# Kernel optimization log

Hardware: AMD Instinct MI355X
Metric: run time of the kernel (lower is better)

The kernel has to match this reference:

```python
import jax, jax.numpy as jnp
import numpy as np

S_DIM, I_DIM, O_DIM = 1024, 2048, 1024
TOTAL = S_DIM + I_DIM + O_DIM  # 4096
INPUT_DIM, NUM_CLASSES, BATCH = 2048, 1000, 256


def setup_inputs() -> dict:
    key = jax.random.key(0)
    ks = jax.random.split(key, 6)
    x = jax.random.normal(ks[0], (BATCH, INPUT_DIM), dtype=jnp.float32)
    W = jax.random.normal(ks[1], (TOTAL, TOTAL), dtype=jnp.float32) * 0.02
    # torch Linear: weight [out, in], bias [out]
    in_w = jax.random.normal(ks[2], (S_DIM, INPUT_DIM), dtype=jnp.float32) * (1.0 / np.sqrt(INPUT_DIM))
    in_b = jax.random.normal(ks[3], (S_DIM,), dtype=jnp.float32) * 0.01
    out_w = jax.random.normal(ks[4], (NUM_CLASSES, O_DIM), dtype=jnp.float32) * (1.0 / np.sqrt(O_DIM))
    out_b = jax.random.normal(ks[5], (NUM_CLASSES,), dtype=jnp.float32) * 0.01
    return {"x": x, "W": W, "in_w": in_w, "in_b": in_b, "out_w": out_w, "out_b": out_b, "time_steps": 10}


def reference(x, W, in_w, in_b, out_w, out_b, time_steps):
    B = x.shape[0]
    S, I, O = S_DIM, I_DIM, O_DIM
    # slice effective W into 9 sub-blocks (use_lora=False -> W_eff = W)
    W_ss, W_sr, W_so = W[:S, :S], W[:S, S:S + I], W[:S, S + I:]
    W_rs, W_rr, W_ro = W[S:S + I, :S], W[S:S + I, S:S + I], W[S:S + I, S + I:]
    W_os, W_or, W_oo = W[S + I:, :S], W[S + I:, S:S + I], W[S + I:, S + I:]

    E = x @ in_w.T + in_b  # [B, S]
    gate = (jnp.arange(time_steps) % 5 == 0).astype(x.dtype)  # E injected when t%5==0

    init = (jnp.zeros((B, S), x.dtype), jnp.zeros((B, I), x.dtype), jnp.zeros((B, O), x.dtype))

    def step(carry, g):
        Ss, Is, Os = carry
        S_next = jax.nn.relu(Ss @ W_ss + g * E + Is @ W_rs + Os @ W_os)
        I_next = jax.nn.relu(Is @ W_rr + Ss @ W_sr + Os @ W_or)
        O_next = jax.nn.relu(Os @ W_oo + Is @ W_ro + Ss @ W_so)
        return (S_next, I_next, O_next), None

    (Ss, Is, Os), _ = jax.lax.scan(step, init, gate)
    return Os @ out_w.T + out_b  # [B, num_classes]
```

## Files before the change

### kernel.cpp

```cpp
#include <hip/hip_runtime.h>


typedef __bf16 bf16x8 __attribute__((ext_vector_type(8)));
typedef float  f32x16 __attribute__((ext_vector_type(16)));

#define TOTAL 4096
#define BATCH 256
#define INDIM 2048
#define SDIM  1024
#define NCLS  1000

#define MFMA(a, b, c) __builtin_amdgcn_mfma_f32_32x32x16_bf16((a), (b), (c), 0, 0, 0)

__device__ inline f32x16 zero16() {
    f32x16 v;
#pragma unroll
    for (int i = 0; i < 16; ++i) v[i] = 0.f;
    return v;
}

__device__ inline void swz_slot(const float* __restrict__ in, __bf16* __restrict__ out,
                                int C, int Rvalid, int t) {
    const int lane = t & 63;
    const int frag = t >> 6;
    const int kcN = C >> 4;
    const int rt = frag / kcN;
    const int kc = frag - rt * kcN;
    const int r = rt * 32 + (lane & 31);
    const int c = kc * 16 + (lane >> 5) * 8;
    alignas(16) __bf16 v[8];
    if (r < Rvalid) {
        const float* p = in + (size_t)r * C + c;
#pragma unroll
        for (int j = 0; j < 8; ++j) v[j] = (__bf16)p[j];
    } else {
#pragma unroll
        for (int j = 0; j < 8; ++j) v[j] = (__bf16)0.f;
    }
    *(ulonglong2*)(out + (size_t)t * 8) = *(const ulonglong2*)v;
}

__global__ __launch_bounds__(256) void k_prep(const float* __restrict__ W,
                                              const float* __restrict__ x,
                                              const float* __restrict__ in_w,
                                              const float* __restrict__ in_b,
                                              const float* __restrict__ out_w,
                                              __bf16* __restrict__ WT,
                                              __bf16* __restrict__ OWT,
                                              float* __restrict__ Ebuf,
                                              __bf16* __restrict__ H0) {
    __shared__ float t[16 * 512];
    const int bid = blockIdx.x;
    const int tid = threadIdx.x;
    if (bid < 256) {
        float* red = t;
        const int mt = bid >> 5, nt = bid & 31;
        const int wave = tid >> 6, lane = tid & 63;
        const int l31 = lane & 31, kh = (lane >> 5) * 8;
        const int k0 = wave * 512;
        const float* Ax = x    + (size_t)(mt * 32 + l31) * INDIM + k0 + kh;
        const float* Bw = in_w + (size_t)(nt * 32 + l31) * INDIM + k0 + kh;
        f32x16 acc = zero16();
#pragma unroll 4
        for (int i = 0; i < 32; ++i) {
            const float* pa = Ax + i * 16;
            const float* pb = Bw + i * 16;
            float4 a0 = *(const float4*)pa, a1 = *(const float4*)(pa + 4);
            float4 b0 = *(const float4*)pb, b1 = *(const float4*)(pb + 4);
            bf16x8 a, b;
            a[0] = (__bf16)a0.x; a[1] = (__bf16)a0.y; a[2] = (__bf16)a0.z; a[3] = (__bf16)a0.w;
            a[4] = (__bf16)a1.x; a[5] = (__bf16)a1.y; a[6] = (__bf16)a1.z; a[7] = (__bf16)a1.w;
            b[0] = (__bf16)b0.x; b[1] = (__bf16)b0.y; b[2] = (__bf16)b0.z; b[3] = (__bf16)b0.w;
            b[4] = (__bf16)b1.x; b[5] = (__bf16)b1.y; b[6] = (__bf16)b1.z; b[7] = (__bf16)b1.w;
            acc = MFMA(a, b, acc);
        }
#pragma unroll
        for (int r = 0; r < 16; ++r) {
            int row = (r & 3) + 8 * (r >> 2) + 4 * (lane >> 5);
            red[wave * 1024 + row * 32 + l31] = acc[r];
        }
        __syncthreads();
        const int e0 = tid * 4;
        float4 s = {0.f, 0.f, 0.f, 0.f};
#pragma unroll
        for (int w = 0; w < 4; ++w) {
            float4 v = *(const float4*)&red[w * 1024 + e0];
            s.x += v.x; s.y += v.y; s.z += v.z; s.w += v.w;
        }
        const int row = e0 >> 5, col = e0 & 31;
        const int m = mt * 32 + row, n = nt * 32 + col;
        float v[4] = {s.x + in_b[n], s.y + in_b[n + 1], s.z + in_b[n + 2], s.w + in_b[n + 3]};
        *(float4*)(Ebuf + m * SDIM + n) = *(const float4*)v;
        alignas(8) __bf16 o[4];
#pragma unroll
        for (int j = 0; j < 4; ++j) o[j] = (__bf16)fmaxf(v[j], 0.f);
        const size_t frag = (size_t)(m >> 5) * (TOTAL / 16) + (n >> 4);
        const int lh = (m & 31) + 32 * ((n >> 3) & 1);
        *(ushort4*)(H0 + frag * 512 + lh * 8 + (n & 7)) = *(const ushort4*)o;
    } else if (bid < 2304) {
        const int wb = bid - 256;
        const int k0 = (wb >> 3) * 16;
        const int n0 = (wb & 7) * 512;
#pragma unroll
        for (int i = 0; i < 8; ++i) {
            const int slot = i * 256 + tid;
            const int row = slot >> 7;
            const int c4 = (slot & 127) * 4;
            float4 v = *(const float4*)(W + (size_t)(k0 + row) * TOTAL + n0 + c4);
            *(float4*)&t[row * 512 + c4] = v;
        }
        __syncthreads();
        const int kcG = k0 >> 4;
#pragma unroll
        for (int s = tid; s < 1024; s += 256) {
            const int rtl = s >> 6;
            const int lane = s & 63;
            const int nl = rtl * 32 + (lane & 31);
            const int kl = (lane >> 5) * 8;
            bf16x8 v;
#pragma unroll
            for (int j = 0; j < 8; ++j) v[j] = (__bf16)t[(kl + j) * 512 + nl];
            const size_t fragG = (size_t)((n0 >> 5) + rtl) * (TOTAL / 16) + kcG;
            *(bf16x8*)(WT + fragG * 512 + lane * 8) = v;
        }
    } else {
        swz_slot(out_w, OWT, 1024, NCLS, (bid - 2304) * 256 + tid);
    }
}

template <int CHUNKS>
__global__ __launch_bounds__(1024, 1) void k_step3(const __bf16* __restrict__ h,
                                                   const __bf16* __restrict__ WT,
                                                   const float* __restrict__ E,
                                                   const int gate,
                                                   __bf16* __restrict__ hn) {
    __shared__ float buf[8][4096];
    const int w = threadIdx.x >> 6;
    const int lane = threadIdx.x & 63;
    const int xcd = blockIdx.x & 7;
    const int idx = blockIdx.x >> 3;
    const int mt = idx & 3;
    const int nt = xcd * 8 + (idx >> 2);
    constexpr int PER = CHUNKS >> 4;
    const int kc0 = w * PER;

    const bf16x8* A0 = (const bf16x8*)h  + ((size_t)(mt * 2) * (TOTAL / 16) + kc0) * 64 + lane;
    const bf16x8* A1 = A0 + (size_t)(TOTAL / 16) * 64;
    const bf16x8* B0 = (const bf16x8*)WT + ((size_t)(nt * 2) * (TOTAL / 16) + kc0) * 64 + lane;
    const bf16x8* B1 = B0 + (size_t)(TOTAL / 16) * 64;

    f32x16 ac0 = zero16(), ac1 = zero16(), ac2 = zero16(), ac3 = zero16();
#pragma unroll 4
    for (int i = 0; i < PER; ++i) {
        const int off = i * 64;
        bf16x8 a0 = A0[off];
        bf16x8 a1 = A1[off];
        bf16x8 b0 = B0[off];
        bf16x8 b1 = B1[off];
        ac0 = MFMA(a0, b0, ac0);
        ac1 = MFMA(a0, b1, ac1);
        ac2 = MFMA(a1, b0, ac2);
        ac3 = MFMA(a1, b1, ac3);
    }

    f32x16 accs[4] = {ac0, ac1, ac2, ac3};
    if (w >= 8) {
        float* b = buf[w - 8];
#pragma unroll
        for (int cc = 0; cc < 4; ++cc)
#pragma unroll
            for (int rr = 0; rr < 16; ++rr)
                b[(cc * 16 + rr) * 64 + lane] = accs[cc][rr];
    }
    __syncthreads();
    if (w < 8) {
        float* b = buf[w];
#pragma unroll
        for (int cc = 0; cc < 4; ++cc)
#pragma unroll
            for (int rr = 0; rr < 16; ++rr) {
                const int i2 = (cc * 16 + rr) * 64 + lane;
                b[i2] += accs[cc][rr];
            }
    }
    __syncthreads();

    const int t = threadIdx.x;
    const int c = t >> 8;
    const int r = (t >> 4) & 15;
    const int l0 = (t & 15) * 4;
    const int base = (c * 16 + r) * 64 + l0;
    float4 s = {0.f, 0.f, 0.f, 0.f};
#pragma unroll
    for (int wb = 0; wb < 8; ++wb) {
        float4 v0 = *(const float4*)&buf[wb][base];
        s.x += v0.x; s.y += v0.y; s.z += v0.z; s.w += v0.w;
    }
    float v[4] = {s.x, s.y, s.z, s.w};
    const int ih = c >> 1, jh = c & 1;
    const int row = ih * 32 + (r & 3) + 8 * (r >> 2) + 4 * (l0 >> 5);
    const int col0 = jh * 32 + (l0 & 31);
    const int m = mt * 64 + row;
    const int n0g = nt * 64 + col0;
    if (gate && n0g < SDIM) {
        const float* Ep = E + m * SDIM + n0g;
#pragma unroll
        for (int j = 0; j < 4; ++j) v[j] += Ep[j];
    }
    alignas(8) __bf16 o[4];
#pragma unroll
    for (int j = 0; j < 4; ++j) o[j] = (__bf16)fmaxf(v[j], 0.f);
    const size_t frag = (size_t)(m >> 5) * (TOTAL / 16) + (n0g >> 4);
    const int lh = (m & 31) + 32 * ((n0g >> 3) & 1);
    *(ushort4*)(hn + frag * 512 + lh * 8 + (n0g & 7)) = *(const ushort4*)o;
}

__global__ __launch_bounds__(512, 2) void k_part9(const __bf16* __restrict__ h,
                                                  const __bf16* __restrict__ WT,
                                                  float* __restrict__ P) {
    __shared__ float buf[4][4096];
    const int wave = threadIdx.x >> 6;
    const int lane = threadIdx.x & 63;
    const int xcd = blockIdx.x & 7;
    const int idx = blockIdx.x >> 3;
    const int nt = 48 + xcd * 2 + (idx >> 4);
    const int mt = (idx >> 2) & 3;
    const int ks = idx & 3;
    const int kc0 = ks * 64 + wave * 8;

    const bf16x8* A0 = (const bf16x8*)h  + ((size_t)(mt * 2) * (TOTAL / 16) + kc0) * 64 + lane;
    const bf16x8* A1 = A0 + (size_t)(TOTAL / 16) * 64;
    const bf16x8* B0 = (const bf16x8*)WT + ((size_t)(nt * 2) * (TOTAL / 16) + kc0) * 64 + lane;
    const bf16x8* B1 = B0 + (size_t)(TOTAL / 16) * 64;

    f32x16 ac0 = zero16(), ac1 = zero16(), ac2 = zero16(), ac3 = zero16();
#pragma unroll 4
    for (int i = 0; i < 8; ++i) {
        const int off = i * 64;
        bf16x8 a0 = A0[off];
        bf16x8 a1 = A1[off];
        bf16x8 b0 = B0[off];
        bf16x8 b1 = B1[off];
        ac0 = MFMA(a0, b0, ac0);
        ac1 = MFMA(a0, b1, ac1);
        ac2 = MFMA(a1, b0, ac2);
        ac3 = MFMA(a1, b1, ac3);
    }

    f32x16 accs[4] = {ac0, ac1, ac2, ac3};
    if (wave >= 4) {
        float* b = buf[wave - 4];
#pragma unroll
        for (int c = 0; c < 4; ++c)
#pragma unroll
            for (int r = 0; r < 16; ++r)
                b[(c * 16 + r) * 64 + lane] = accs[c][r];
    }
    __syncthreads();
    if (wave < 4) {
        float* b = buf[wave];
#pragma unroll
        for (int c = 0; c < 4; ++c)
#pragma unroll
            for (int r = 0; r < 16; ++r) {
                const int i2 = (c * 16 + r) * 64 + lane;
                b[i2] += accs[c][r];
            }
    }
    __syncthreads();

    const int t = threadIdx.x;
    const int c = t >> 7;
    const int r = (t >> 3) & 15;
    const int l0 = (t & 7) * 8;
    const int base = (c * 16 + r) * 64 + l0;
    float4 s0 = {0.f, 0.f, 0.f, 0.f}, s1 = {0.f, 0.f, 0.f, 0.f};
#pragma unroll
    for (int w = 0; w < 4; ++w) {
        const float4* p = (const float4*)&buf[w][base];
        float4 v0 = p[0], v1 = p[1];
        s0.x += v0.x; s0.y += v0.y; s0.z += v0.z; s0.w += v0.w;
        s1.x += v1.x; s1.y += v1.y; s1.z += v1.z; s1.w += v1.w;
    }
    alignas(16) float v[8] = {s0.x, s0.y, s0.z, s0.w, s1.x, s1.y, s1.z, s1.w};
    const int ih = c >> 1, jh = c & 1;
    const int row = ih * 32 + (r & 3) + 8 * (r >> 2) + 4 * (l0 >> 5);
    const int col0 = jh * 32 + (l0 & 31);
    const int m = mt * 64 + row;
    const int nl = (nt - 48) * 64 + col0;
    float* p = P + ((size_t)ks << 18) + (size_t)m * 1024 + nl;
    *(float4*)p = *(const float4*)&v[0];
    *(float4*)(p + 4) = *(const float4*)&v[4];
}

__global__ __launch_bounds__(256) void k_red9(const float* __restrict__ P,
                                              __bf16* __restrict__ hn) {
    const int g = blockIdx.x * 256 + threadIdx.x;
    const int m = g >> 7;
    const int n8 = (g & 127) << 3;
    const float* p = P + (size_t)m * 1024 + n8;
    float4 a0 = *(const float4*)p, a1 = *(const float4*)(p + 4);
#pragma unroll
    for (int ks = 1; ks < 4; ++ks) {
        const float* q = p + ((size_t)ks << 18);
        float4 b0 = *(const float4*)q, b1 = *(const float4*)(q + 4);
        a0.x += b0.x; a0.y += b0.y; a0.z += b0.z; a0.w += b0.w;
        a1.x += b1.x; a1.y += b1.y; a1.z += b1.z; a1.w += b1.w;
    }
    alignas(16) __bf16 o[8];
    o[0] = (__bf16)fmaxf(a0.x, 0.f); o[1] = (__bf16)fmaxf(a0.y, 0.f);
    o[2] = (__bf16)fmaxf(a0.z, 0.f); o[3] = (__bf16)fmaxf(a0.w, 0.f);
    o[4] = (__bf16)fmaxf(a1.x, 0.f); o[5] = (__bf16)fmaxf(a1.y, 0.f);
    o[6] = (__bf16)fmaxf(a1.z, 0.f); o[7] = (__bf16)fmaxf(a1.w, 0.f);
    const int n0g = 3072 + n8;
    const size_t frag = (size_t)(m >> 5) * (TOTAL / 16) + (n0g >> 4);
    const int lh = (m & 31) + 32 * ((n0g >> 3) & 1);
    *(ulonglong2*)(hn + frag * 512 + lh * 8) = *(const ulonglong2*)o;
}

__global__ __launch_bounds__(512, 4) void k_out(const __bf16* __restrict__ h,
                                                const __bf16* __restrict__ owt,
                                                const float* __restrict__ out_b,
                                                float* __restrict__ out) {
    __shared__ float red[8][1024];
    const int wave = threadIdx.x >> 6;
    const int lane = threadIdx.x & 63;
    const int mt = blockIdx.x >> 5;
    const int ct = blockIdx.x & 31;
    const int m0 = mt * 32, c0 = ct * 32;
    const int kcA0 = (3072 / 16) + wave * 8;
    const int kcB0 = wave * 8;
    const bf16x8* Ap = (const bf16x8*)h   + ((size_t)mt * (TOTAL / 16) + kcA0) * 64 + lane;
    const bf16x8* Bp = (const bf16x8*)owt + ((size_t)ct * (1024 / 16) + kcB0) * 64 + lane;
    f32x16 acc = zero16();
#pragma unroll
    for (int i = 0; i < 8; ++i)
        acc = MFMA(Ap[i * 64], Bp[i * 64], acc);
#pragma unroll
    for (int r = 0; r < 16; ++r) {
        int row = (r & 3) + 8 * (r >> 2) + 4 * (lane >> 5);
        red[wave][row * 32 + (lane & 31)] = acc[r];
    }
    __syncthreads();
    const int e0 = threadIdx.x * 2;
    float sx = 0.f, sy = 0.f;
#pragma unroll
    for (int w = 0; w < 8; ++w) {
        float2 v = *(const float2*)&red[w][e0];
        sx += v.x; sy += v.y;
    }
    const int row = e0 >> 5, col = e0 & 31;
    const int m = m0 + row;
    const int n = c0 + col;
    if (n < NCLS)     out[m * NCLS + n]     = sx + out_b[n];
    if (n + 1 < NCLS) out[m * NCLS + n + 1] = sy + out_b[n + 1];
}

extern "C" void kernel_launch(void* const* d_in, const int* in_sizes, int n_in,
                              void* d_out, int out_size, void* d_ws, size_t ws_size,
                              hipStream_t stream) {
    const float* x     = (const float*)d_in[0];
    const float* W     = (const float*)d_in[1];
    const float* in_w  = (const float*)d_in[2];
    const float* in_b  = (const float*)d_in[3];
    const float* out_w = (const float*)d_in[4];
    const float* out_b = (const float*)d_in[5];
    float* out = (float*)d_out;

    char* ws = (char*)d_ws;
    __bf16* WT  = (__bf16*)(ws + 0);
    __bf16* OWT = (__bf16*)(ws + 33554432);
    float*  Ebuf= (float*)(ws + 35651584);
    __bf16* H0  = (__bf16*)(ws + 36700160);
    __bf16* H1  = (__bf16*)(ws + 38797312);
    float*  Pbuf= (float*)(ws + 40894464);

    k_prep<<<2816, 256, 0, stream>>>(W, x, in_w, in_b, out_w, WT, OWT, Ebuf, H0);

    const __bf16* hs = H0;
    __bf16* hd = H1;
    for (int t = 1; t < 9; ++t) {
        const int gate = (t % 5 == 0) ? 1 : 0;
        if (t == 1)
            k_step3<SDIM / 16><<<256, 1024, 0, stream>>>(hs, WT, Ebuf, gate, hd);
        else
            k_step3<TOTAL / 16><<<256, 1024, 0, stream>>>(hs, WT, Ebuf, gate, hd);
        const __bf16* tmp = hs; hs = hd; hd = (__bf16*)tmp;
    }

    k_part9<<<256, 512, 0, stream>>>(hs, WT, Pbuf);
    k_red9<<<128, 256, 0, stream>>>(Pbuf, hd);

    k_out<<<256, 512, 0, stream>>>(hd, OWT, out_b, out);
}
```

Measured before the change: 257.6 us.

## Replace full recurrent steps with split-K partial GEMM plus reduction kernel

For steps 2-8, the single fused k_step3 kernel is replaced by a split-K GEMM (k_partF, 4 K-slices, 128x128 tiles over 256 blocks) that writes fp32 partials, followed by a separate reduction kernel that sums the partials, adds the gated input, applies ReLU and writes the bf16 fragment layout. The goal is more parallelism and better occupancy across the machine for a 256x4096x4096 GEMM per step. In exchange, each step writes and rereads a 16 MB fp32 partial buffer and adds an extra launch.

New measurement: 422.8 us. +64.1%, slower.

```diff
diff --git a/kernel.cpp b/kernel.cpp
--- a/kernel.cpp
+++ b/kernel.cpp
@@ -215,6 +215,80 @@
     *(ushort4*)(hn + frag * 512 + lh * 8 + (n0g & 7)) = *(const ushort4*)o;
 }
 
+__global__ __launch_bounds__(512, 2) void k_partF(const __bf16* __restrict__ h,
+                                                  const __bf16* __restrict__ WT,
+                                                  float* __restrict__ P) {
+    const int w = threadIdx.x >> 6;
+    const int lane = threadIdx.x & 63;
+    const int xcd = blockIdx.x & 7;
+    const int idx = blockIdx.x >> 3;
+    const int nt = xcd * 4 + (idx & 3);
+    const int ks = (idx >> 2) & 3;
+    const int mt = idx >> 4;
+    const int wm = w & 1, wn = w >> 1;
+    const int fA = mt * 4 + wm * 2;
+    const int fB = nt * 4 + wn;
+    const int kc0 = ks * 64;
+
+    const bf16x8* A0 = (const bf16x8*)h  + ((size_t)fA * (TOTAL / 16) + kc0) * 64 + lane;
+    const bf16x8* A1 = A0 + (size_t)(TOTAL / 16) * 64;
+    const bf16x8* B0 = (const bf16x8*)WT + ((size_t)fB * (TOTAL / 16) + kc0) * 64 + lane;
+
+    f32x16 ac0 = zero16(), ac1 = zero16();
+#pragma unroll 4
+    for (int i = 0; i < 64; ++i) {
+        const int off = i * 64;
+        bf16x8 a0 = A0[off];
+        bf16x8 a1 = A1[off];
+        bf16x8 b  = B0[off];
+        ac0 = MFMA(a0, b, ac0);
+        ac1 = MFMA(a1, b, ac1);
+    }
+
+    const int m0 = mt * 128 + wm * 64;
+    const int n0 = nt * 128 + wn * 32 + (lane & 31);
+    const int rb = 4 * (lane >> 5);
+    float* Pp = P + (size_t)ks * (BATCH * TOTAL) + (size_t)m0 * TOTAL + n0;
+#pragma unroll
+    for (int r = 0; r < 16; ++r) {
+        const int row = (r & 3) + 8 * (r >> 2) + rb;
+        Pp[(size_t)row * TOTAL] = ac0[r];
+        Pp[(size_t)(row + 32) * TOTAL] = ac1[r];
+    }
+}
+
+__global__ __launch_bounds__(256) void k_red2(const float* __restrict__ P,
+                                              const float* __restrict__ E,
+                                              const int gate,
+                                              __bf16* __restrict__ hn) {
+    const int g = blockIdx.x * 256 + threadIdx.x;
+    const int m = g >> 9;
+    const int n8 = (g & 511) << 3;
+    const float* p = P + (size_t)m * TOTAL + n8;
+    float4 a0 = *(const float4*)p, a1 = *(const float4*)(p + 4);
+#pragma unroll
+    for (int s = 1; s < 4; ++s) {
+        const float* q = p + (size_t)s * (BATCH * TOTAL);
+        float4 b0 = *(const float4*)q, b1 = *(const float4*)(q + 4);
+        a0.x += b0.x; a0.y += b0.y; a0.z += b0.z; a0.w += b0.w;
+        a1.x += b1.x; a1.y += b1.y; a1.z += b1.z; a1.w += b1.w;
+    }
+    if (gate && n8 < SDIM) {
+        const float* Ep = E + (size_t)m * SDIM + n8;
+        float4 e0 = *(const float4*)Ep, e1 = *(const float4*)(Ep + 4);
+        a0.x += e0.x; a0.y += e0.y; a0.z += e0.z; a0.w += e0.w;
+        a1.x += e1.x; a1.y += e1.y; a1.z += e1.z; a1.w += e1.w;
+    }
+    alignas(16) __bf16 o[8];
+    o[0] = (__bf16)fmaxf(a0.x, 0.f); o[1] = (__bf16)fmaxf(a0.y, 0.f);
+    o[2] = (__bf16)fmaxf(a0.z, 0.f); o[3] = (__bf16)fmaxf(a0.w, 0.f);
+    o[4] = (__bf16)fmaxf(a1.x, 0.f); o[5] = (__bf16)fmaxf(a1.y, 0.f);
+    o[6] = (__bf16)fmaxf(a1.z, 0.f); o[7] = (__bf16)fmaxf(a1.w, 0.f);
+    const size_t frag = (size_t)(m >> 5) * (TOTAL / 16) + (n8 >> 4);
+    const int lh = (m & 31) + 32 * ((n8 >> 3) & 1);
+    *(ulonglong2*)(hn + frag * 512 + lh * 8) = *(const ulonglong2*)o;
+}
+
 __global__ __launch_bounds__(512, 2) void k_part9(const __bf16* __restrict__ h,
                                                   const __bf16* __restrict__ WT,
                                                   float* __restrict__ P) {
@@ -379,12 +453,13 @@
 
     const __bf16* hs = H0;
     __bf16* hd = H1;
-    for (int t = 1; t < 9; ++t) {
-        const int gate = (t % 5 == 0) ? 1 : 0;
-        if (t == 1)
-            k_step3<SDIM / 16><<<256, 1024, 0, stream>>>(hs, WT, Ebuf, gate, hd);
-        else
-            k_step3<TOTAL / 16><<<256, 1024, 0, stream>>>(hs, WT, Ebuf, gate, hd);
+
+    k_step3<SDIM / 16><<<256, 1024, 0, stream>>>(hs, WT, Ebuf, 0, hd);
+    { const __bf16* tmp = hs; hs = hd; hd = (__bf16*)tmp; }
+
+    for (int t = 2; t < 9; ++t) {
+        k_partF<<<256, 512, 0, stream>>>(hs, WT, Pbuf);
+        k_red2<<<512, 256, 0, stream>>>(Pbuf, Ebuf, (t % 5 == 0) ? 1 : 0, hd);
         const __bf16* tmp = hs; hs = hd; hd = (__bf16*)tmp;
     }
 
```
